# Kernel optimization log

Measured on AMD Instinct MI355X. Metric: run time of the kernel, lower is better.

The kernel has to match this reference:

```python
import jax, jax.numpy as jnp
import numpy as np

INPUT_DIM = 1024
HIDDEN_DIM = 2048
LATENT_DIM = 256
NUM_EMBEDDINGS = 8192
COMMITMENT_COST = 0.25
BATCH = 16384


def setup_inputs() -> dict:
    key = jax.random.key(0)
    ks = jax.random.split(key, 10)
    def lin(k, fan_in, fan_out):
        # torch nn.Linear default init: U(-1/sqrt(fan_in), 1/sqrt(fan_in))
        bound = 1.0 / np.sqrt(fan_in)
        kw, kb = jax.random.split(k)
        W = jax.random.uniform(kw, (fan_in, fan_out), jnp.float32, -bound, bound)
        b = jax.random.uniform(kb, (fan_out,), jnp.float32, -bound, bound)
        return W, b
    enc_w1, enc_b1 = lin(ks[0], INPUT_DIM, HIDDEN_DIM)
    enc_w2, enc_b2 = lin(ks[1], HIDDEN_DIM, LATENT_DIM)
    dec_w1, dec_b1 = lin(ks[2], LATENT_DIM, HIDDEN_DIM)
    dec_w2, dec_b2 = lin(ks[3], HIDDEN_DIM, INPUT_DIM)
    # codebook init: U(-1/K, 1/K)
    codebook = jax.random.uniform(ks[4], (NUM_EMBEDDINGS, LATENT_DIM), jnp.float32,
                                  -1.0 / NUM_EMBEDDINGS, 1.0 / NUM_EMBEDDINGS)
    x = jax.random.uniform(ks[5], (BATCH, INPUT_DIM), jnp.float32)
    return {"x": x,
            "enc_w1": enc_w1, "enc_b1": enc_b1, "enc_w2": enc_w2, "enc_b2": enc_b2,
            "codebook": codebook,
            "dec_w1": dec_w1, "dec_b1": dec_b1, "dec_w2": dec_w2, "dec_b2": dec_b2}


def reference(x, enc_w1, enc_b1, enc_w2, enc_b2, codebook,
              dec_w1, dec_b1, dec_w2, dec_b2):
    # Encoder: relu(x W1 + b1) W2 + b2 -> z [N, latent]
    h = jax.nn.relu(x @ enc_w1 + enc_b1)
    z = h @ enc_w2 + enc_b2

    # Vector quantizer: squared-L2 distances to codebook [N, K]
    d = (jnp.sum(z * z, axis=1, keepdims=True)
         + jnp.sum(codebook * codebook, axis=1)
         - 2.0 * (z @ codebook.T))
    idx = jnp.argmin(d, axis=1)          # [N] int
    z_q = codebook[idx]                   # gather [N, latent]

    vq_loss = jnp.mean((jax.lax.stop_gradient(z_q) - z) ** 2)
    commit_loss = COMMITMENT_COST * jnp.mean((z_q - jax.lax.stop_gradient(z)) ** 2)
    loss = vq_loss + commit_loss

    # straight-through estimator
    z_q = z + jax.lax.stop_gradient(z_q - z)

    # Decoder: sigmoid(relu(z_q Wd1 + bd1) Wd2 + bd2)
    hd = jax.nn.relu(z_q @ dec_w1 + dec_b1)
    x_recon = jax.nn.sigmoid(hd @ dec_w2 + dec_b2)
    return (x_recon, loss)
```

## Files before the change

kernel.cpp:

```cpp
#include <hip/hip_runtime.h>
#include <math.h>

typedef unsigned short u16;
typedef __bf16 bf16x8 __attribute__((ext_vector_type(8)));
typedef float  f32x4  __attribute__((ext_vector_type(4)));

constexpr int B_  = 16384;
constexpr int DIN = 1024;
constexpr int DH  = 2048;
constexpr int DL  = 256;
constexpr int NE  = 8192;

__device__ __forceinline__ u16 f2bf(float f) {
    union { float f; unsigned u; } v; v.f = f;
    unsigned r = v.u + 0x7fffu + ((v.u >> 16) & 1u);
    return (u16)(r >> 16);
}
__device__ __forceinline__ float bf2f(u16 h) {
    union { unsigned u; float f; } v; v.u = ((unsigned)h) << 16;
    return v.f;
}

#define GLD16(gp, lp)                                                  \
    __builtin_amdgcn_global_load_lds(                                  \
        (__attribute__((address_space(1))) void*)(gp),                 \
        (__attribute__((address_space(3))) void*)(lp), 16, 0, 0)

#define SCHED0() __builtin_amdgcn_sched_barrier(0)
#define BARRIER() do { SCHED0(); __builtin_amdgcn_s_barrier(); SCHED0(); } while (0)
#define WAITV0() asm volatile("s_waitcnt vmcnt(0)" ::: "memory")
#define WAITV3() asm volatile("s_waitcnt vmcnt(3)" ::: "memory")
#define WAITV4() asm volatile("s_waitcnt vmcnt(4)" ::: "memory")

__global__ __launch_bounds__(256)
void cast_bf16(const float* __restrict__ in, u16* __restrict__ out)
{
    const size_t i = ((size_t)blockIdx.x * 256 + threadIdx.x) * 4;
    float4 v = *(const float4*)(in + i);
    ushort4 o;
    o.x = f2bf(v.x); o.y = f2bf(v.y); o.z = f2bf(v.z); o.w = f2bf(v.w);
    *(ushort4*)(out + i) = o;
}

__global__ __launch_bounds__(256)
void transpose_cast(const float* __restrict__ in, u16* __restrict__ out,
                    int R, int C)
{
    __shared__ float t[32][33];
    const int tx = threadIdx.x & 31, ty = threadIdx.x >> 5;
    const long bx = blockIdx.x;
    const long by = blockIdx.y;
#pragma unroll
    for (int p = 0; p < 4; ++p)
        t[ty + p * 8][tx] = in[(by * 32 + ty + p * 8) * (long)C + bx * 32 + tx];
    __syncthreads();
#pragma unroll
    for (int p = 0; p < 4; ++p)
        out[(bx * 32 + ty + p * 8) * (long)R + by * 32 + tx] = f2bf(t[tx][ty + p * 8]);
}

__global__ __launch_bounds__(256)
void cn2_kernel(const float* __restrict__ cb, float* __restrict__ cn2)
{
    const int code = (blockIdx.x * 256 + threadIdx.x) >> 6;
    const int lane = threadIdx.x & 63;
    float4 v = *(const float4*)(cb + (long)code * DL + lane * 4);
    float s = fmaf(v.x, v.x, fmaf(v.y, v.y, fmaf(v.z, v.z, v.w * v.w)));
#pragma unroll
    for (int off = 32; off; off >>= 1) s += __shfl_down(s, off);
    if (lane == 0) cn2[code] = 0.5f * s;
}

template <int EPI>
__global__ __launch_bounds__(512, 4)
void gemm_big_bf16(const u16* __restrict__ A, const u16* __restrict__ Bt,
                   const float* __restrict__ bias, void* __restrict__ Cout,
                   int M, int N, int K)
{
    __shared__ __align__(16) u16 As[3 * 8192];
    __shared__ __align__(16) u16 Bs[3 * 4096];

    const int tid = threadIdx.x;
    const int w = tid >> 6, l = tid & 63;
    const int wm = w >> 1, wn = w & 1;

    const int nbx   = N >> 7;
    const int nwg   = (M >> 8) * nbx;
    const int chunk = nwg >> 3;
    const int wg    = ((int)blockIdx.x & 7) * chunk + ((int)blockIdx.x >> 3);
    const long by   = wg / nbx;
    const long bx   = wg % nbx;

    const int lr  = l >> 2;
    const int lsw = (l & 3) ^ ((l >> 3) & 3);
    const int lg  = l >> 4, lm = l & 15;
    const int sx  = (lm >> 1) & 3;

    const u16* Abase = A  + (size_t)(by * 256) * K;
    const u16* Bbase = Bt + (size_t)(bx * 128) * K;

    f32x4 acc[4][4] = {};

    auto stage = [&](int k0, int b) {
        u16* dA = As + b * 8192;
        u16* dB = Bs + b * 4096;
#pragma unroll
        for (int i = 0; i < 2; ++i) {
            const int seg = w * 2 + i;
            GLD16(Abase + (size_t)(seg * 16 + lr) * K + k0 + lsw * 8,
                  dA + seg * 512);
        }
        GLD16(Bbase + (size_t)(w * 16 + lr) * K + k0 + lsw * 8,
              dB + w * 512);
    };

    const int NT = K >> 5;
    stage(0, 0);
    stage(32, 1);

    int cur = 0, pre = 2;
    for (int t = 0; t < NT; ++t) {
        if (t + 1 < NT) { WAITV3(); } else { WAITV0(); }
        BARRIER();
        if (t + 2 < NT) stage((t + 2) << 5, pre);

        const u16* as = As + cur * 8192;
        const u16* bs = Bs + cur * 4096;
        bf16x8 af[4], bfr[4];
#pragma unroll
        for (int m = 0; m < 4; ++m) {
            const int R = wm * 64 + m * 16 + lm;
            af[m] = *(const bf16x8*)&as[R * 32 + ((lg ^ sx) * 8)];
        }
#pragma unroll
        for (int n = 0; n < 4; ++n) {
            const int R = wn * 64 + n * 16 + lm;
            bfr[n] = *(const bf16x8*)&bs[R * 32 + ((lg ^ sx) * 8)];
        }
#pragma unroll
        for (int m = 0; m < 4; ++m)
#pragma unroll
            for (int n = 0; n < 4; ++n)
                acc[m][n] = __builtin_amdgcn_mfma_f32_16x16x32_bf16(
                    af[m], bfr[n], acc[m][n], 0, 0, 0);

        cur = (cur == 2) ? 0 : cur + 1;
        pre = (pre == 2) ? 0 : pre + 1;
    }

#pragma unroll
    for (int n = 0; n < 4; ++n) {
        const long col = bx * 128 + wn * 64 + n * 16 + lm;
        const float bb = bias[col];
#pragma unroll
        for (int m = 0; m < 4; ++m) {
#pragma unroll
            for (int j = 0; j < 4; ++j) {
                const long row = by * 256 + wm * 64 + m * 16 + lg * 4 + j;
                float e = acc[m][n][j] + bb;
                if (EPI == 1) e = fmaxf(e, 0.f);
                if (EPI == 2) {
                    e = 1.f / (1.f + expf(-e));
                    ((float*)Cout)[row * (long)N + col] = e;
                } else {
                    ((u16*)Cout)[row * (long)N + col] = f2bf(e);
                }
            }
        }
    }
}

template <int EPI>
__global__ __launch_bounds__(256)
void gemm_bt_bf16(const u16* __restrict__ A, const u16* __restrict__ Bt,
                  const float* __restrict__ bias, void* __restrict__ Cout,
                  int M, int N, int K)
{
    __shared__ __align__(16) u16 As[3 * 4096];
    __shared__ __align__(16) u16 Bs[3 * 4096];

    const int tid = threadIdx.x;
    const int w = tid >> 6, l = tid & 63;
    const int wr = w >> 1, wc = w & 1;

    const int nbx   = N >> 7;
    const int nwg   = (M >> 7) * nbx;
    const int chunk = nwg >> 3;
    const int wg    = ((int)blockIdx.x & 7) * chunk + ((int)blockIdx.x >> 3);
    const long by   = wg / nbx;
    const long bx   = wg % nbx;

    const int lr  = l >> 2;
    const int lsw = (l & 3) ^ ((l >> 3) & 3);
    const int lg  = l >> 4, lm = l & 15;
    const int sx  = (lm >> 1) & 3;

    const u16* Abase = A  + (size_t)(by * 128) * K;
    const u16* Bbase = Bt + (size_t)(bx * 128) * K;

    f32x4 acc[4][4] = {};

    auto stage = [&](int k0, int b) {
        u16* dA = As + b * 4096;
        u16* dB = Bs + b * 4096;
#pragma unroll
        for (int i = 0; i < 2; ++i) {
            const int seg = w * 2 + i;
            GLD16(Abase + (size_t)(seg * 16 + lr) * K + k0 + lsw * 8, dA + seg * 512);
            GLD16(Bbase + (size_t)(seg * 16 + lr) * K + k0 + lsw * 8, dB + seg * 512);
        }
    };

    const int NT = K >> 5;
    stage(0, 0);
    stage(32, 1);

    int cur = 0, pre = 2;
    for (int t = 0; t < NT; ++t) {
        if (t + 1 < NT) { WAITV4(); } else { WAITV0(); }
        BARRIER();
        if (t + 2 < NT) stage((t + 2) << 5, pre);

        const u16* as = As + cur * 4096;
        const u16* bs = Bs + cur * 4096;
        bf16x8 af[4], bfr[4];
#pragma unroll
        for (int m = 0; m < 4; ++m)
            af[m] = *(const bf16x8*)&as[(wr * 64 + m * 16 + lm) * 32 + ((lg ^ sx) * 8)];
#pragma unroll
        for (int n = 0; n < 4; ++n)
            bfr[n] = *(const bf16x8*)&bs[(wc * 64 + n * 16 + lm) * 32 + ((lg ^ sx) * 8)];
#pragma unroll
        for (int m = 0; m < 4; ++m)
#pragma unroll
            for (int n = 0; n < 4; ++n)
                acc[m][n] = __builtin_amdgcn_mfma_f32_16x16x32_bf16(
                    af[m], bfr[n], acc[m][n], 0, 0, 0);

        cur = (cur == 2) ? 0 : cur + 1;
        pre = (pre == 2) ? 0 : pre + 1;
    }

#pragma unroll
    for (int n = 0; n < 4; ++n) {
        const long col = bx * 128 + wc * 64 + n * 16 + lm;
        const float bb = bias[col];
#pragma unroll
        for (int m = 0; m < 4; ++m) {
#pragma unroll
            for (int j = 0; j < 4; ++j) {
                const long row = by * 128 + wr * 64 + m * 16 + lg * 4 + j;
                float e = acc[m][n][j] + bb;
                if (EPI == 1) e = fmaxf(e, 0.f);
                if (EPI == 2) {
                    e = 1.f / (1.f + expf(-e));
                    ((float*)Cout)[row * (long)N + col] = e;
                } else {
                    ((u16*)Cout)[row * (long)N + col] = f2bf(e);
                }
            }
        }
    }
}

__global__ __launch_bounds__(256, 2)
void vq_score2(const u16* __restrict__ z, const u16* __restrict__ cbt,
               const float* __restrict__ cn2,
               float* __restrict__ val8, int* __restrict__ idx8)
{
    __shared__ __align__(16) u16 lds[32768];

    const int tid = threadIdx.x;
    const int w = tid >> 6, l = tid & 63;
    const int rq = blockIdx.x >> 3;
    const int q  = blockIdx.x & 7;

    const int st_row8 = tid >> 5;
    const int st_s    = (tid & 31) ^ st_row8;
    const int lg = l >> 4, lm = l & 15;
    const int swz_x = l & 7;

    bf16x8 af[4][8];
    const long zbase_row = (long)rq * 256;
#pragma unroll
    for (int h = 0; h < 2; ++h) {
#pragma unroll
        for (int i = 0; i < 16; ++i) {
            const int row = i * 8 + st_row8;
            const u16* g = z + (zbase_row + h * 128 + row) * DL + st_s * 8;
            GLD16(g, lds + ((size_t)i * 256 + w * 64) * 8);
        }
        __syncthreads();
        if ((w >> 1) == h) {
            const int lrow0 = (w & 1) * 64;
#pragma unroll
            for (int m = 0; m < 4; ++m) {
                const int lrow = lrow0 + m * 16 + lm;
#pragma unroll
                for (int kg = 0; kg < 8; ++kg) {
                    const int s = (kg * 4 + lg) ^ swz_x;
                    af[m][kg] = *(const bf16x8*)&lds[lrow * 256 + s * 8];
                }
            }
        }
        __syncthreads();
    }

    const int code00 = q * (NE / 8);

    float bestv[16];
    int   besti[16];
#pragma unroll
    for (int k = 0; k < 16; ++k) { bestv[k] = 1e30f; besti[k] = 0; }

    auto stage_tile = [&](int t) {
        const int b = t & 1;
#pragma unroll
        for (int i = 0; i < 8; ++i) {
            const int c = i * 8 + st_row8;
            const u16* g = cbt + (size_t)(code00 + t * 64 + c) * DL + st_s * 8;
            GLD16(g, lds + ((size_t)b * 16384 + ((size_t)i * 256 + w * 64) * 8));
        }
    };

    stage_tile(0);
    __syncthreads();

    for (int t = 0; t < 16; ++t) {
        if (t < 15) stage_tile(t + 1);
        const u16* buf = lds + (size_t)(t & 1) * 16384;

#pragma unroll
        for (int n = 0; n < 4; ++n) {
            const int code_g = code00 + t * 64 + n * 16 + lm;
            const float cn2v = cn2[code_g];
            bf16x8 bfr[8];
#pragma unroll
            for (int kg = 0; kg < 8; ++kg) {
                const int lrow = n * 16 + lm;
                const int s = (kg * 4 + lg) ^ swz_x;
                bfr[kg] = *(const bf16x8*)&buf[lrow * 256 + s * 8];
            }
            f32x4 acc[4] = {};
#pragma unroll
            for (int kg = 0; kg < 8; ++kg)
#pragma unroll
                for (int m = 0; m < 4; ++m)
                    acc[m] = __builtin_amdgcn_mfma_f32_16x16x32_bf16(
                        af[m][kg], bfr[kg], acc[m], 0, 0, 0);
#pragma unroll
            for (int m = 0; m < 4; ++m)
#pragma unroll
                for (int j = 0; j < 4; ++j) {
                    const float s = cn2v - acc[m][j];
                    const int k16 = m * 4 + j;
                    if (s < bestv[k16]) { bestv[k16] = s; besti[k16] = code_g; }
                }
        }
        __syncthreads();
    }

#pragma unroll
    for (int off = 1; off < 16; off <<= 1) {
#pragma unroll
        for (int k = 0; k < 16; ++k) {
            const float ov = __shfl_xor(bestv[k], off);
            const int   oi = __shfl_xor(besti[k], off);
            if (ov < bestv[k] || (ov == bestv[k] && oi < besti[k])) {
                bestv[k] = ov; besti[k] = oi;
            }
        }
    }
    if (lm == 0) {
#pragma unroll
        for (int m = 0; m < 4; ++m)
#pragma unroll
            for (int j = 0; j < 4; ++j) {
                const long row = zbase_row + w * 64 + m * 16 + lg * 4 + j;
                val8[(size_t)q * B_ + row] = bestv[m * 4 + j];
                idx8[(size_t)q * B_ + row] = besti[m * 4 + j];
            }
    }
}

__global__ __launch_bounds__(256)
void vq_select2(const float* __restrict__ val8, const int* __restrict__ idx8,
                const u16* __restrict__ z, const float* __restrict__ cb,
                int* __restrict__ idxf, float* __restrict__ partial)
{
    __shared__ int   s_idx[256];
    __shared__ float s_red[4];
    const int tid = threadIdx.x;
    const long row = (long)blockIdx.x * 256 + tid;

    float bv = val8[row];
    int   bi = idx8[row];
#pragma unroll
    for (int qq = 1; qq < 8; ++qq) {
        const float v = val8[(size_t)qq * B_ + row];
        const int   i = idx8[(size_t)qq * B_ + row];
        if (v < bv || (v == bv && i < bi)) { bv = v; bi = i; }
    }
    s_idx[tid] = bi;
    idxf[row]  = bi;
    __syncthreads();

    float ls = 0.f;
    const int sub = tid & 7;
#pragma unroll
    for (int pass = 0; pass < 8; ++pass) {
        const int rl = pass * 32 + (tid >> 3);
        const int gi = s_idx[rl];
        const long rg = (long)blockIdx.x * 256 + rl;
#pragma unroll
        for (int tt = 0; tt < 8; ++tt) {
            const int d = sub * 4 + tt * 32;
            float4 c4 = *(const float4*)(cb + (long)gi * DL + d);
            ushort4 zu = *(const ushort4*)(z + rg * DL + d);
            const float dx = c4.x - bf2f(zu.x), dy = c4.y - bf2f(zu.y);
            const float dz = c4.z - bf2f(zu.z), dw = c4.w - bf2f(zu.w);
            ls += dx * dx + dy * dy + dz * dz + dw * dw;
        }
    }
#pragma unroll
    for (int off = 32; off; off >>= 1) ls += __shfl_down(ls, off);
    if ((tid & 63) == 0) s_red[tid >> 6] = ls;
    __syncthreads();
    if (tid == 0)
        partial[blockIdx.x] = s_red[0] + s_red[1] + s_red[2] + s_red[3];
}

__global__ __launch_bounds__(256)
void loss_finalize(const float* __restrict__ partial, float* __restrict__ out)
{
    __shared__ float s_red[4];
    const int tid = threadIdx.x;
    float s = (tid < 64) ? partial[tid] : 0.f;
#pragma unroll
    for (int off = 32; off; off >>= 1) s += __shfl_down(s, off);
    if ((tid & 63) == 0) s_red[tid >> 6] = s;
    __syncthreads();
    if (tid == 0)
        out[0] = 1.25f * (s_red[0] + s_red[1] + s_red[2] + s_red[3])
                 / (float)((long)B_ * DL);
}

__global__ __launch_bounds__(256)
void gather_rows(const float* __restrict__ Xcode, const int* __restrict__ idxf,
                 float* __restrict__ out)
{
    const int tid  = threadIdx.x;
    const int lane = tid & 63;
    const long row = (long)blockIdx.x * 4 + (tid >> 6);
    const long gi  = idxf[row];
    const float* src = Xcode + gi * DIN;
    float*       dst = out + row * DIN;
#pragma unroll
    for (int t = 0; t < 4; ++t) {
        const int d = lane * 4 + t * 256;
        *(float4*)(dst + d) = *(const float4*)(src + d);
    }
}

extern "C" void kernel_launch(void* const* d_in, const int* in_sizes, int n_in,
                              void* d_out, int out_size, void* d_ws, size_t ws_size,
                              hipStream_t stream)
{
    const float* x   = (const float*)d_in[0];
    const float* ew1 = (const float*)d_in[1];
    const float* eb1 = (const float*)d_in[2];
    const float* ew2 = (const float*)d_in[3];
    const float* eb2 = (const float*)d_in[4];
    const float* cbk = (const float*)d_in[5];
    const float* dw1 = (const float*)d_in[6];
    const float* db1 = (const float*)d_in[7];
    const float* dw2 = (const float*)d_in[8];
    const float* db2 = (const float*)d_in[9];
    float* out = (float*)d_out;

    char* p = (char*)d_ws;
    auto alloc = [&](size_t bytes) {
        char* r = p; p += (bytes + 255) & ~(size_t)255; return r;
    };
    u16*   x_bf  = (u16*)alloc((size_t)B_ * DIN * 2);
    u16*   h_bf  = (u16*)alloc((size_t)B_ * DH * 2);
    u16*   z_bf  = (u16*)alloc((size_t)B_ * DL * 2);
    u16*   cb_bf = (u16*)alloc((size_t)NE * DL * 2);
    u16*   w1t   = (u16*)alloc((size_t)DH * DIN * 2);
    u16*   w2t   = (u16*)alloc((size_t)DL * DH * 2);
    u16*   wd1t  = (u16*)alloc((size_t)DH * DL * 2);
    u16*   wd2t  = (u16*)alloc((size_t)DIN * DH * 2);
    float* Xcode = (float*)alloc((size_t)NE * DIN * 4);
    float* cn2   = (float*)alloc((size_t)NE * 4);
    float* val8  = (float*)alloc((size_t)8 * B_ * 4);
    int*   idx8  = (int*)alloc((size_t)8 * B_ * 4);
    int*   idxf  = (int*)alloc((size_t)B_ * 4);
    float* part  = (float*)alloc(64 * 4);

    cast_bf16<<<(size_t)B_ * DIN / 1024, 256, 0, stream>>>(x, x_bf);
    cast_bf16<<<(size_t)NE * DL / 1024, 256, 0, stream>>>(cbk, cb_bf);
    transpose_cast<<<dim3(DH / 32, DIN / 32), 256, 0, stream>>>(ew1, w1t, DIN, DH);
    transpose_cast<<<dim3(DL / 32, DH / 32), 256, 0, stream>>>(ew2, w2t, DH, DL);
    transpose_cast<<<dim3(DH / 32, DL / 32), 256, 0, stream>>>(dw1, wd1t, DL, DH);
    transpose_cast<<<dim3(DIN / 32, DH / 32), 256, 0, stream>>>(dw2, wd2t, DH, DIN);
    cn2_kernel<<<NE / 4, 256, 0, stream>>>(cbk, cn2);

    gemm_big_bf16<1><<<(B_ / 256) * (DH / 128), 512, 0, stream>>>(
        x_bf, w1t, eb1, h_bf, B_, DH, DIN);
    gemm_bt_bf16<0><<<(B_ / 128) * (DL / 128), 256, 0, stream>>>(
        h_bf, w2t, eb2, z_bf, B_, DL, DH);

    vq_score2<<<512, 256, 0, stream>>>(z_bf, cb_bf, cn2, val8, idx8);
    vq_select2<<<B_ / 256, 256, 0, stream>>>(val8, idx8, z_bf, cbk, idxf, part);
    loss_finalize<<<1, 256, 0, stream>>>(part, out + (size_t)B_ * DIN);

    gemm_big_bf16<1><<<(NE / 256) * (DH / 128), 512, 0, stream>>>(
        cb_bf, wd1t, db1, h_bf, NE, DH, DL);
    gemm_big_bf16<2><<<(NE / 256) * (DIN / 128), 512, 0, stream>>>(
        h_bf, wd2t, db2, Xcode, NE, DIN, DH);
    gather_rows<<<B_ / 4, 256, 0, stream>>>(Xcode, idxf, out);
}
```

Before: 324.7 us.

## Deepen GEMM LDS pipeline to four stages with prefetch-after-fragment-load schedule

The big bf16 GEMM moves from a 3-buffer to a 4-buffer LDS ring and prefetches three K-tiles ahead. The loop now reads LDS fragments first, issues the next global-to-LDS load, waits on lgkmcnt, and raises wave priority around the MFMA block. It adds a barrier at both the start and end of each iteration. The goal is to hide global-load latency better and overlap loads with MFMA work. In exchange, the larger LDS footprint lowers occupancy (launch bounds drop from 4 to 2 blocks per CU) and each iteration pays an extra barrier.

```diff
diff --git a/kernel.cpp b/kernel.cpp
--- a/kernel.cpp
+++ b/kernel.cpp
@@ -31,6 +31,8 @@
 #define WAITV0() asm volatile("s_waitcnt vmcnt(0)" ::: "memory")
 #define WAITV3() asm volatile("s_waitcnt vmcnt(3)" ::: "memory")
 #define WAITV4() asm volatile("s_waitcnt vmcnt(4)" ::: "memory")
+#define WAITV6() asm volatile("s_waitcnt vmcnt(6)" ::: "memory")
+#define WAITLG0() do { asm volatile("s_waitcnt lgkmcnt(0)" ::: "memory"); SCHED0(); } while (0)
 
 __global__ __launch_bounds__(256)
 void cast_bf16(const float* __restrict__ in, u16* __restrict__ out)
@@ -72,13 +74,13 @@
 }
 
 template <int EPI>
-__global__ __launch_bounds__(512, 4)
-void gemm_big_bf16(const u16* __restrict__ A, const u16* __restrict__ Bt,
+__global__ __launch_bounds__(512, 2)
+void gemm_8ph_bf16(const u16* __restrict__ A, const u16* __restrict__ Bt,
                    const float* __restrict__ bias, void* __restrict__ Cout,
                    int M, int N, int K)
 {
-    __shared__ __align__(16) u16 As[3 * 8192];
-    __shared__ __align__(16) u16 Bs[3 * 4096];
+    __shared__ __align__(16) u16 As[4 * 8192];
+    __shared__ __align__(16) u16 Bs[4 * 4096];
 
     const int tid = threadIdx.x;
     const int w = tid >> 6, l = tid & 63;
@@ -101,7 +103,9 @@
 
     f32x4 acc[4][4] = {};
 
-    auto stage = [&](int k0, int b) {
+    auto stage = [&](int t) {
+        const int b  = t & 3;
+        const int k0 = t << 5;
         u16* dA = As + b * 8192;
         u16* dB = Bs + b * 4096;
 #pragma unroll
@@ -115,17 +119,13 @@
     };
 
     const int NT = K >> 5;
-    stage(0, 0);
-    stage(32, 1);
-
-    int cur = 0, pre = 2;
+    stage(0); stage(1); stage(2);
+    WAITV6();
+    BARRIER();
+
     for (int t = 0; t < NT; ++t) {
-        if (t + 1 < NT) { WAITV3(); } else { WAITV0(); }
-        BARRIER();
-        if (t + 2 < NT) stage((t + 2) << 5, pre);
-
-        const u16* as = As + cur * 8192;
-        const u16* bs = Bs + cur * 4096;
+        const u16* as = As + (t & 3) * 8192;
+        const u16* bs = Bs + (t & 3) * 4096;
         bf16x8 af[4], bfr[4];
 #pragma unroll
         for (int m = 0; m < 4; ++m) {
@@ -137,15 +137,23 @@
             const int R = wn * 64 + n * 16 + lm;
             bfr[n] = *(const bf16x8*)&bs[R * 32 + ((lg ^ sx) * 8)];
         }
+        if (t + 3 < NT) stage(t + 3);
+
+        BARRIER();
+        WAITLG0();
+        __builtin_amdgcn_s_setprio(1);
 #pragma unroll
         for (int m = 0; m < 4; ++m)
 #pragma unroll
             for (int n = 0; n < 4; ++n)
                 acc[m][n] = __builtin_amdgcn_mfma_f32_16x16x32_bf16(
                     af[m], bfr[n], acc[m][n], 0, 0, 0);
-
-        cur = (cur == 2) ? 0 : cur + 1;
-        pre = (pre == 2) ? 0 : pre + 1;
+        __builtin_amdgcn_s_setprio(0);
+
+        if (t + 3 < NT)      { WAITV6(); }
+        else if (t + 2 < NT) { WAITV3(); }
+        else                 { WAITV0(); }
+        BARRIER();
     }
 
 #pragma unroll
@@ -505,7 +513,7 @@
     transpose_cast<<<dim3(DIN / 32, DH / 32), 256, 0, stream>>>(dw2, wd2t, DH, DIN);
     cn2_kernel<<<NE / 4, 256, 0, stream>>>(cbk, cn2);
 
-    gemm_big_bf16<1><<<(B_ / 256) * (DH / 128), 512, 0, stream>>>(
+    gemm_8ph_bf16<1><<<(B_ / 256) * (DH / 128), 512, 0, stream>>>(
         x_bf, w1t, eb1, h_bf, B_, DH, DIN);
     gemm_bt_bf16<0><<<(B_ / 128) * (DL / 128), 256, 0, stream>>>(
         h_bf, w2t, eb2, z_bf, B_, DL, DH);
@@ -514,9 +522,9 @@
     vq_select2<<<B_ / 256, 256, 0, stream>>>(val8, idx8, z_bf, cbk, idxf, part);
     loss_finalize<<<1, 256, 0, stream>>>(part, out + (size_t)B_ * DIN);
 
-    gemm_big_bf16<1><<<(NE / 256) * (DH / 128), 512, 0, stream>>>(
+    gemm_8ph_bf16<1><<<(NE / 256) * (DH / 128), 512, 0, stream>>>(
         cb_bf, wd1t, db1, h_bf, NE, DH, DL);
-    gemm_big_bf16<2><<<(NE / 256) * (DIN / 128), 512, 0, stream>>>(
+    gemm_8ph_bf16<2><<<(NE / 256) * (DIN / 128), 512, 0, stream>>>(
         h_bf, wd2t, db2, Xcode, NE, DIN, DH);
     gather_rows<<<B_ / 4, 256, 0, stream>>>(Xcode, idxf, out);
 }
```

Measured after the change: 330.0 us. About the same (+1.6%).
